# Optimization experiments

Hardware: AMD Instinct MI355X
Metric: run time of the kernel (lower is better)

Reference implementation:

```python
import jax, jax.numpy as jnp
import numpy as np

WS = 6        # window size -> N = 36 tokens per window
HEADS = 16

def _rel_index(ws):
    coords = np.stack(np.meshgrid(np.arange(ws), np.arange(ws), indexing='ij')).reshape(2, -1)
    rel = coords[:, :, None] - coords[:, None, :] + (ws - 1)
    return jnp.asarray(rel[0] * (2 * ws - 1) + rel[1])  # (N, N) int

REL_IDX = _rel_index(WS)

def _ln(x, g, b, eps=1e-5):
    m = x.mean(-1, keepdims=True)
    v = x.var(-1, keepdims=True)
    return (x - m) / jnp.sqrt(v + eps) * g + b

def setup_inputs() -> dict:
    key = jax.random.key(0)
    ks = jax.random.split(key, 6)
    B, H, W, C = 16, 96, 96, 512
    hid = 4 * C
    s = 0.02
    return {
        'x': jax.random.normal(ks[0], (B, H, W, C), jnp.float32),
        'w_qkv': jax.random.normal(ks[1], (C, 3 * C), jnp.float32) * s,
        'w_proj': jax.random.normal(ks[2], (C, C), jnp.float32) * s,
        'b_proj': jnp.zeros((C,), jnp.float32),
        'rel_bias': jax.random.normal(ks[3], ((2 * WS - 1) ** 2, HEADS), jnp.float32) * s,
        'ln1_g': jnp.ones((C,), jnp.float32), 'ln1_b': jnp.zeros((C,), jnp.float32),
        'ln2_g': jnp.ones((C,), jnp.float32), 'ln2_b': jnp.zeros((C,), jnp.float32),
        'w_fc1': jax.random.normal(ks[4], (C, hid), jnp.float32) * s,
        'b_fc1': jnp.zeros((hid,), jnp.float32),
        'w_fc2': jax.random.normal(ks[5], (hid, C), jnp.float32) * s,
        'b_fc2': jnp.zeros((C,), jnp.float32),
    }

def reference(x, w_qkv, w_proj, b_proj, rel_bias, ln1_g, ln1_b, ln2_g, ln2_b, w_fc1, b_fc1, w_fc2, b_fc2):
    B, H, W, C = x.shape
    h, d, N = HEADS, C // HEADS, WS * WS
    nh, nw = H // WS, W // WS
    # window partition: (B,H,W,C) -> (B*nh*nw, N, C)
    xw = x.reshape(B, nh, WS, nw, WS, C).transpose(0, 1, 3, 2, 4, 5).reshape(B * nh * nw, N, C)
    xn = _ln(xw, ln1_g, ln1_b)
    qkv = xn @ w_qkv
    q, k, v = jnp.split(qkv, 3, axis=-1)
    to_heads = lambda t: t.reshape(-1, N, h, d).transpose(0, 2, 1, 3)  # (B_, h, N, d)
    q = to_heads(q) * (d ** -0.5)
    k = to_heads(k)
    v = to_heads(v)
    attn = jnp.einsum('bhnd,bhmd->bhnm', q, k)
    bias = rel_bias[REL_IDX.reshape(-1)].reshape(N, N, h).transpose(2, 0, 1)  # (h, N, N)
    attn = jax.nn.softmax(attn + bias[None], axis=-1)
    o = jnp.einsum('bhnm,bhmd->bhnd', attn, v).transpose(0, 2, 1, 3).reshape(-1, N, C)
    o = o @ w_proj + b_proj
    # un-window; NOTE: source has no residual around attention (x is replaced)
    x2 = o.reshape(B, nh, nw, WS, WS, C).transpose(0, 1, 3, 2, 4, 5).reshape(B, H, W, C)
    xm = _ln(x2, ln2_g, ln2_b)
    mlp = jax.nn.gelu(xm @ w_fc1 + b_fc1, approximate=False) @ w_fc2 + b_fc2
    return x2 + mlp
```

## Files before the change

kernel.cpp:

```cpp
#include <hip/hip_runtime.h>
#include <stdint.h>

#define TOK 147456
#define CCH 512

typedef __attribute__((ext_vector_type(8))) short short8;
typedef __attribute__((ext_vector_type(4))) float f32x4;

struct alignas(8) US4 { unsigned short a, b, c, d; };

typedef __attribute__((address_space(3))) void lds_void;
typedef const __attribute__((address_space(1))) void gbl_void;

__device__ inline void gload16(const void* g, void* l) {
    __builtin_amdgcn_global_load_lds((gbl_void*)g, (lds_void*)l, 16, 0, 0);
}

__device__ inline unsigned short f2bf(float f) {
    union { float f; unsigned u; } v{f};
    unsigned r = v.u + 0x7fffu + ((v.u >> 16) & 1u);
    return (unsigned short)(r >> 16);
}
__device__ inline float bf2f(unsigned short h) {
    union { unsigned u; float f; } v; v.u = ((unsigned)h) << 16; return v.f;
}
__device__ inline float frcp(float x) {
    float r; asm("v_rcp_f32 %0, %1" : "=v"(r) : "v"(x)); return r;
}

__global__ void wprep(const float* __restrict__ in, unsigned short* __restrict__ out,
                      int K, int N) {
    int idx = blockIdx.x * 256 + threadIdx.x;
    if (idx >= K * N) return;
    int k = idx / N, n = idx % N;
    out[(size_t)n * K + k] = f2bf(in[idx]);
}

__global__ void biasprep(const float* __restrict__ rb, float* __restrict__ bb) {
    int idx = blockIdx.x * 256 + threadIdx.x;
    if (idx >= 16 * 48 * 48) return;
    int h = idx / 2304, rem = idx % 2304, r = rem / 48, c = rem % 48;
    float v = -1e9f;
    if (r < 36 && c < 36) {
        int dy = r / 6 - c / 6 + 5;
        int dx = r % 6 - c % 6 + 5;
        v = rb[(dy * 11 + dx) * 16 + h];
    }
    bb[idx] = v;
}

__global__ __launch_bounds__(256) void ln_k(const float* __restrict__ x,
                                            const float* __restrict__ g,
                                            const float* __restrict__ b,
                                            unsigned short* __restrict__ out, int ntok) {
    int lane = threadIdx.x & 63;
    int tok = blockIdx.x * 4 + (threadIdx.x >> 6);
    if (tok >= ntok) return;
    const float4* xr = (const float4*)(x + (size_t)tok * CCH);
    float4 v0 = xr[lane], v1 = xr[lane + 64];
    float s  = v0.x + v0.y + v0.z + v0.w + v1.x + v1.y + v1.z + v1.w;
    float s2 = v0.x*v0.x + v0.y*v0.y + v0.z*v0.z + v0.w*v0.w
             + v1.x*v1.x + v1.y*v1.y + v1.z*v1.z + v1.w*v1.w;
#pragma unroll
    for (int off = 32; off; off >>= 1) { s += __shfl_xor(s, off); s2 += __shfl_xor(s2, off); }
    float mean = s * (1.f / 512.f);
    float var  = s2 * (1.f / 512.f) - mean * mean;
    float inv  = rsqrtf(var + 1e-5f);
    const float4* gp = (const float4*)g;
    const float4* bp = (const float4*)b;
    float4 g0 = gp[lane], g1 = gp[lane + 64], b0 = bp[lane], b1 = bp[lane + 64];
    US4 o0, o1;
    o0.a = f2bf((v0.x - mean) * inv * g0.x + b0.x);
    o0.b = f2bf((v0.y - mean) * inv * g0.y + b0.y);
    o0.c = f2bf((v0.z - mean) * inv * g0.z + b0.z);
    o0.d = f2bf((v0.w - mean) * inv * g0.w + b0.w);
    o1.a = f2bf((v1.x - mean) * inv * g1.x + b1.x);
    o1.b = f2bf((v1.y - mean) * inv * g1.y + b1.y);
    o1.c = f2bf((v1.z - mean) * inv * g1.z + b1.z);
    o1.d = f2bf((v1.w - mean) * inv * g1.w + b1.w);
    unsigned short* op = out + (size_t)tok * CCH;
    *(US4*)(op + 4 * lane)       = o0;
    *(US4*)(op + 256 + 4 * lane) = o1;
}

__global__ __launch_bounds__(256) void ln_bf(const unsigned short* __restrict__ x,
                                             const float* __restrict__ g,
                                             const float* __restrict__ b,
                                             unsigned short* __restrict__ out, int ntok) {
    int lane = threadIdx.x & 63;
    int tok = blockIdx.x * 4 + (threadIdx.x >> 6);
    if (tok >= ntok) return;
    short8 v = *(const short8*)(x + (size_t)tok * CCH + lane * 8);
    float f[8];
#pragma unroll
    for (int j = 0; j < 8; ++j) f[j] = bf2f((unsigned short)v[j]);
    float s = 0.f, s2 = 0.f;
#pragma unroll
    for (int j = 0; j < 8; ++j) { s += f[j]; s2 += f[j] * f[j]; }
#pragma unroll
    for (int off = 32; off; off >>= 1) { s += __shfl_xor(s, off); s2 += __shfl_xor(s2, off); }
    float mean = s * (1.f / 512.f);
    float var  = s2 * (1.f / 512.f) - mean * mean;
    float inv  = rsqrtf(var + 1e-5f);
    const float4* gp = (const float4*)g + lane * 2;
    const float4* bp = (const float4*)b + lane * 2;
    float4 g0 = gp[0], g1 = gp[1], b0 = bp[0], b1 = bp[1];
    float gg[8] = {g0.x, g0.y, g0.z, g0.w, g1.x, g1.y, g1.z, g1.w};
    float bb[8] = {b0.x, b0.y, b0.z, b0.w, b1.x, b1.y, b1.z, b1.w};
    short8 o;
#pragma unroll
    for (int j = 0; j < 8; ++j) o[j] = (short)f2bf((f[j] - mean) * inv * gg[j] + bb[j]);
    *(short8*)(out + (size_t)tok * CCH + lane * 8) = o;
}

__global__ __launch_bounds__(256) void attn_mfma(const unsigned short* __restrict__ qkv,
                                                 const float* __restrict__ biasb,
                                                 unsigned short* __restrict__ o) {
    __shared__ __align__(16) unsigned short p_lds[4][48 * 64];
    __shared__ __align__(16) unsigned short v_lds[4][32 * 64];

    int tid  = threadIdx.x;
    int wv   = tid >> 6;
    int lane = tid & 63;
    int l15  = lane & 15;
    int g    = lane >> 4;

    int wid = blockIdx.x * 4 + wv;
    int h   = wid & 15;
    int win = wid >> 4;
    int img  = win >> 8;
    int wrow = (win >> 4) & 15;
    int wcol = win & 15;
    int tok_base = (img * 96 + wrow * 6) * 96 + wcol * 6;

    unsigned short* pw = p_lds[wv];
    unsigned short* vw = v_lds[wv];

    #define TOKOF(r) (tok_base + (r) + 90 * ((r) / 6))

    short8 z8 = {};
    for (int e = lane; e < 224; e += 64) {
        if (e < 128) {
            int ch = e >> 2, kst = 32 + (e & 3) * 8;
            *(short8*)(vw + ch * 64 + (kst ^ ((ch & 7) << 3))) = z8;
        } else {
            int ee = e - 128; int q = ee >> 1, kst = 48 + (ee & 1) * 8;
            *(short8*)(pw + q * 64 + (kst ^ ((q & 7) << 3))) = z8;
        }
    }

    for (int e = lane; e < 144; e += 64) {
        int r = e >> 2, c0 = (e & 3) * 8;
        short8 vv = *(const short8*)(qkv + (size_t)TOKOF(r) * 1536 + 1024 + h * 32 + c0);
#pragma unroll
        for (int j = 0; j < 8; ++j) {
            int ch = c0 + j;
            vw[ch * 64 + (r ^ ((ch & 7) << 3))] = (unsigned short)vv[j];
        }
    }

    short8 qf[3], kf[3];
#pragma unroll
    for (int t = 0; t < 3; ++t) {
        int r = t * 16 + l15;
        if (r < 36) {
            size_t ba = (size_t)TOKOF(r) * 1536 + h * 32 + g * 8;
            qf[t] = *(const short8*)(qkv + ba);
            kf[t] = *(const short8*)(qkv + ba + 512);
        } else { qf[t] = z8; kf[t] = z8; }
    }

    f32x4 s[3][3] = {};
#pragma unroll
    for (int mt = 0; mt < 3; ++mt)
#pragma unroll
        for (int nt = 0; nt < 3; ++nt)
            s[mt][nt] = __builtin_amdgcn_mfma_f32_16x16x32_bf16(qf[mt], kf[nt], s[mt][nt], 0, 0, 0);

    const float SCALE = 0.17677669529663687f;
    const float* bh = biasb + h * 2304;
#pragma unroll
    for (int mt = 0; mt < 3; ++mt) {
#pragma unroll
        for (int r = 0; r < 4; ++r) {
            int row = mt * 16 + g * 4 + r;
            const float* bb = bh + row * 48 + l15;
            float v0 = fmaf(s[mt][0][r], SCALE, bb[0]);
            float v1 = fmaf(s[mt][1][r], SCALE, bb[16]);
            float v2 = fmaf(s[mt][2][r], SCALE, bb[32]);
            float m = fmaxf(fmaxf(v0, v1), v2);
#pragma unroll
            for (int off = 1; off < 16; off <<= 1) m = fmaxf(m, __shfl_xor(m, off));
            float e0 = __expf(v0 - m), e1 = __expf(v1 - m), e2 = __expf(v2 - m);
            float sm = e0 + e1 + e2;
#pragma unroll
            for (int off = 1; off < 16; off <<= 1) sm += __shfl_xor(sm, off);
            float inv = 1.f / sm;
            int sw = (row & 7) << 3;
            unsigned short* pr = pw + row * 64;
            pr[(l15)      ^ sw] = f2bf(e0 * inv);
            pr[(16 + l15) ^ sw] = f2bf(e1 * inv);
            pr[(32 + l15) ^ sw] = f2bf(e2 * inv);
        }
    }

    f32x4 oacc[3][2] = {};
#pragma unroll
    for (int ks = 0; ks < 2; ++ks) {
        int kst = ks * 32 + g * 8;
        short8 bfr[2];
#pragma unroll
        for (int nt = 0; nt < 2; ++nt) {
            int c = nt * 16 + l15;
            bfr[nt] = *(const short8*)(vw + c * 64 + (kst ^ ((c & 7) << 3)));
        }
#pragma unroll
        for (int mt = 0; mt < 3; ++mt) {
            int q = mt * 16 + l15;
            short8 pa = *(const short8*)(pw + q * 64 + (kst ^ ((q & 7) << 3)));
#pragma unroll
            for (int nt = 0; nt < 2; ++nt)
                oacc[mt][nt] = __builtin_amdgcn_mfma_f32_16x16x32_bf16(pa, bfr[nt], oacc[mt][nt], 0, 0, 0);
        }
    }

#pragma unroll
    for (int mt = 0; mt < 3; ++mt) {
#pragma unroll
        for (int r = 0; r < 4; ++r) {
            int q = mt * 16 + g * 4 + r;
            if (q < 36) {
                size_t rb = (size_t)TOKOF(q) * 512 + h * 32;
#pragma unroll
                for (int nt = 0; nt < 2; ++nt)
                    o[rb + nt * 16 + l15] = f2bf(oacc[mt][nt][r]);
            }
        }
    }
    #undef TOKOF
}

template <int EPI>
__global__ __launch_bounds__(256, 4) void gemm8(const unsigned short* __restrict__ A,
                                                const unsigned short* __restrict__ Bt,
                                                int M, int N, int K,
                                                const float* __restrict__ bias,
                                                const unsigned short* __restrict__ resid,
                                                void* __restrict__ Cout) {
    extern __shared__ char lds[];
    int tid = threadIdx.x;
    int w = tid >> 6, lane = tid & 63;
    int l15 = lane & 15, grp = lane >> 4;
    int wm = w >> 1, wn = w & 1;

    int nbn = N >> 7;
    int nwg = gridDim.x;
    int q = nwg >> 3, r = nwg & 7;
    int xcd = blockIdx.x & 7, pos_ = blockIdx.x >> 3;
    int wgid = (xcd < r ? xcd * (q + 1) : r * (q + 1) + (xcd - r) * q) + pos_;
    int bm = wgid / nbn, bn = wgid % nbn;

    int NT = K >> 5;

    int u = (tid & 7) ^ ((tid >> 3) & 7);
    int srow = ((tid >> 3) << 1) + (u >> 2);
    int scol = (u & 3) * 8;
    const unsigned short* aSrc = A  + ((size_t)bm * 128 + srow) * (size_t)K + scol;
    const unsigned short* bSrc = Bt + ((size_t)bn * 128 + srow) * (size_t)K + scol;

    #define STAGE(t, sp) do { size_t ko_ = (size_t)(t) * 32; \
        gload16(aSrc + ko_,                  (sp) + tid * 16); \
        gload16(aSrc + ko_ + (size_t)64 * K, (sp) + 4096  + tid * 16); \
        gload16(bSrc + ko_,                  (sp) + 8192  + tid * 16); \
        gload16(bSrc + ko_ + (size_t)64 * K, (sp) + 12288 + tid * 16); } while (0)

    int rpos = (grp + (l15 & 1) * 4) ^ ((l15 >> 1) & 7);
    int aRd = (wm * 32 + (l15 >> 1)) * 128 + rpos * 16;
    int bRd = 8192 + (wn * 32 + (l15 >> 1)) * 128 + rpos * 16;

    f32x4 acc[4][4] = {};

    char* s0 = lds;
    char* s1 = lds + 16384;
    STAGE(0, s0);

    for (int t = 0; t < NT; ++t) {
        char* cur = (t & 1) ? s1 : s0;
        char* nxt = (t & 1) ? s0 : s1;
        if (t + 1 < NT) {
            STAGE(t + 1, nxt);
            asm volatile("s_waitcnt vmcnt(4)" ::: "memory");
        } else {
            asm volatile("s_waitcnt vmcnt(0)" ::: "memory");
        }
        __builtin_amdgcn_s_barrier();
        short8 af[4], bf[4];
#pragma unroll
        for (int m = 0; m < 4; ++m) af[m] = *(const short8*)(cur + aRd + m * 1024);
#pragma unroll
        for (int n = 0; n < 4; ++n) bf[n] = *(const short8*)(cur + bRd + n * 1024);
        asm volatile("s_waitcnt lgkmcnt(0)" ::: "memory");
        __builtin_amdgcn_sched_barrier(0);
        __builtin_amdgcn_s_setprio(1);
#pragma unroll
        for (int m = 0; m < 4; ++m)
#pragma unroll
            for (int n = 0; n < 4; ++n)
                acc[m][n] = __builtin_amdgcn_mfma_f32_16x16x32_bf16(af[m], bf[n], acc[m][n], 0, 0, 0);
        __builtin_amdgcn_s_setprio(0);
        __builtin_amdgcn_s_barrier();
    }
    #undef STAGE

    int row0 = bm * 128 + wm * 64 + grp * 4;
    int col0 = bn * 128 + wn * 64 + l15;
#pragma unroll
    for (int m = 0; m < 4; ++m) {
#pragma unroll
        for (int n = 0; n < 4; ++n) {
            int col = col0 + n * 16;
            float bv = (EPI == 0) ? 0.f : bias[col];
#pragma unroll
            for (int r2 = 0; r2 < 4; ++r2) {
                int row = row0 + m * 16 + r2;
                size_t idx = (size_t)row * N + col;
                float val = acc[m][n][r2] + bv;
                if (EPI == 0) {
                    ((unsigned short*)Cout)[idx] = f2bf(val);
                } else if (EPI == 1) {
                    ((unsigned short*)Cout)[idx] = f2bf(val);
                } else if (EPI == 2) {
                    float t1 = val * val;
                    float t2 = fmaf(t1, 0.0713548163f, 1.5957691216f);
                    float z  = val * t2;
                    float e  = __expf(z);
                    float rr = frcp(e + 1.f);
                    float ge = val - val * rr;
                    ((unsigned short*)Cout)[idx] = f2bf(ge);
                } else {
                    ((float*)Cout)[idx] = val + bf2f(resid[idx]);
                }
            }
        }
    }
}

extern "C" void kernel_launch(void* const* d_in, const int* in_sizes, int n_in,
                              void* d_out, int out_size, void* d_ws, size_t ws_size,
                              hipStream_t stream) {
    const float* x       = (const float*)d_in[0];
    const float* w_qkv   = (const float*)d_in[1];
    const float* w_proj  = (const float*)d_in[2];
    const float* b_proj  = (const float*)d_in[3];
    const float* relb    = (const float*)d_in[4];
    const float* ln1g    = (const float*)d_in[5];
    const float* ln1b    = (const float*)d_in[6];
    const float* ln2g    = (const float*)d_in[7];
    const float* ln2b    = (const float*)d_in[8];
    const float* w_fc1   = (const float*)d_in[9];
    const float* b_fc1   = (const float*)d_in[10];
    const float* w_fc2   = (const float*)d_in[11];
    const float* b_fc2   = (const float*)d_in[12];
    float* out = (float*)d_out;

    hipFuncSetAttribute(reinterpret_cast<const void*>(&gemm8<0>),
                        hipFuncAttributeMaxDynamicSharedMemorySize, 32768);
    hipFuncSetAttribute(reinterpret_cast<const void*>(&gemm8<1>),
                        hipFuncAttributeMaxDynamicSharedMemorySize, 32768);
    hipFuncSetAttribute(reinterpret_cast<const void*>(&gemm8<2>),
                        hipFuncAttributeMaxDynamicSharedMemorySize, 32768);
    hipFuncSetAttribute(reinterpret_cast<const void*>(&gemm8<3>),
                        hipFuncAttributeMaxDynamicSharedMemorySize, 32768);

    char* w = (char*)d_ws;
    unsigned short* wT_qkv  = (unsigned short*)w; w += (size_t)1536 * 512 * 2;
    unsigned short* wT_proj = (unsigned short*)w; w += (size_t)512  * 512 * 2;
    unsigned short* wT_fc1  = (unsigned short*)w; w += (size_t)2048 * 512 * 2;
    unsigned short* wT_fc2  = (unsigned short*)w; w += (size_t)512  * 2048 * 2;
    float* biasb            = (float*)w;          w += (size_t)16 * 48 * 48 * 4;
    size_t wbytes = (size_t)(w - (char*)d_ws);

    int nchunk = 16;
    for (int c = 1; c <= 16; c *= 2) {
        size_t tokc = TOK / c;
        if (wbytes + tokc * 6144 <= ws_size) { nchunk = c; break; }
    }
    size_t tokc = TOK / nchunk;
    unsigned short* buf1 = (unsigned short*)w;
    unsigned short* buf2 = (unsigned short*)(w + tokc * 1024);
    unsigned short* buf3 = (unsigned short*)(w + tokc * 5120);

    wprep<<<(512 * 1536 + 255) / 256, 256, 0, stream>>>(w_qkv,  wT_qkv,  512, 1536);
    wprep<<<(512 * 512  + 255) / 256, 256, 0, stream>>>(w_proj, wT_proj, 512, 512);
    wprep<<<(512 * 2048 + 255) / 256, 256, 0, stream>>>(w_fc1,  wT_fc1,  512, 2048);
    wprep<<<(2048 * 512 + 255) / 256, 256, 0, stream>>>(w_fc2,  wT_fc2,  2048, 512);
    biasprep<<<(16 * 48 * 48 + 255) / 256, 256, 0, stream>>>(relb, biasb);

    int Mc = (int)tokc;
    int gm = Mc / 128;
    int imgs = Mc / 9216;

    for (int c = 0; c < nchunk; ++c) {
        size_t toff = (size_t)c * tokc;
        const float* xc = x + toff * CCH;
        float* outc = out + toff * CCH;

        ln_k<<<Mc / 4, 256, 0, stream>>>(xc, ln1g, ln1b, buf1, Mc);
        gemm8<0><<<gm * 12, 256, 32768, stream>>>(buf1, wT_qkv, Mc, 1536, 512,
                                                  nullptr, nullptr, buf2);
        attn_mfma<<<imgs * 1024, 256, 0, stream>>>(buf2, biasb, buf1);
        gemm8<1><<<gm * 4, 256, 32768, stream>>>(buf1, wT_proj, Mc, 512, 512,
                                                 b_proj, nullptr, buf3);
        ln_bf<<<Mc / 4, 256, 0, stream>>>(buf3, ln2g, ln2b, buf1, Mc);
        gemm8<2><<<gm * 16, 256, 32768, stream>>>(buf1, wT_fc1, Mc, 2048, 512,
                                                  b_fc1, nullptr, buf2);
        gemm8<3><<<gm * 4, 256, 32768, stream>>>(buf2, wT_fc2, Mc, 512, 2048,
                                                 b_fc2, buf3, outc);
    }
}
```

Measured before the change: 1.654 ms.

## Rewrite GEMM as 256x256 tile, 8-wave, 8-phase pipelined MFMA kernel

Replaces the 128x128, 4-wave double-buffered GEMM with a 256x256 tile computed by 8 waves. The kernel uses 128 KB of LDS split into two K-halves of 64 each, and its loop is split into eight phases that interleave global_load_lds prefetches with quadrant MFMA blocks. The goal is higher arithmetic intensity per byte loaded and hiding global-load latency behind MFMA work. In exchange, occupancy drops to one workgroup per CU and the grid shrinks, so the smaller GEMMs may be short of parallelism and register pressure from the 8x4 accumulators rises.

```diff
diff --git a/kernel.cpp b/kernel.cpp
--- a/kernel.cpp
+++ b/kernel.cpp
@@ -241,7 +241,7 @@
 }
 
 template <int EPI>
-__global__ __launch_bounds__(256, 4) void gemm8(const unsigned short* __restrict__ A,
+__global__ __launch_bounds__(512, 1) void gemm8(const unsigned short* __restrict__ A,
                                                 const unsigned short* __restrict__ Bt,
                                                 int M, int N, int K,
                                                 const float* __restrict__ bias,
@@ -250,72 +250,108 @@
     extern __shared__ char lds[];
     int tid = threadIdx.x;
     int w = tid >> 6, lane = tid & 63;
-    int l15 = lane & 15, grp = lane >> 4;
-    int wm = w >> 1, wn = w & 1;
-
-    int nbn = N >> 7;
+    int l15 = lane & 15, grp = lane >> 4, l7 = l15 & 7;
+    int wm = w >> 2, wn = w & 3;
+
+    int nbn = N >> 8;
     int nwg = gridDim.x;
     int q = nwg >> 3, r = nwg & 7;
     int xcd = blockIdx.x & 7, pos_ = blockIdx.x >> 3;
     int wgid = (xcd < r ? xcd * (q + 1) : r * (q + 1) + (xcd - r) * q) + pos_;
     int bm = wgid / nbn, bn = wgid % nbn;
 
-    int NT = K >> 5;
-
-    int u = (tid & 7) ^ ((tid >> 3) & 7);
-    int srow = ((tid >> 3) << 1) + (u >> 2);
-    int scol = (u & 3) * 8;
-    const unsigned short* aSrc = A  + ((size_t)bm * 128 + srow) * (size_t)K + scol;
-    const unsigned short* bSrc = Bt + ((size_t)bn * 128 + srow) * (size_t)K + scol;
-
-    #define STAGE(t, sp) do { size_t ko_ = (size_t)(t) * 32; \
-        gload16(aSrc + ko_,                  (sp) + tid * 16); \
-        gload16(aSrc + ko_ + (size_t)64 * K, (sp) + 4096  + tid * 16); \
-        gload16(bSrc + ko_,                  (sp) + 8192  + tid * 16); \
-        gload16(bSrc + ko_ + (size_t)64 * K, (sp) + 12288 + tid * 16); } while (0)
-
-    int rpos = (grp + (l15 & 1) * 4) ^ ((l15 >> 1) & 7);
-    int aRd = (wm * 32 + (l15 >> 1)) * 128 + rpos * 16;
-    int bRd = 8192 + (wn * 32 + (l15 >> 1)) * 128 + rpos * 16;
-
-    f32x4 acc[4][4] = {};
-
-    char* s0 = lds;
-    char* s1 = lds + 16384;
-    STAGE(0, s0);
-
-    for (int t = 0; t < NT; ++t) {
-        char* cur = (t & 1) ? s1 : s0;
-        char* nxt = (t & 1) ? s0 : s1;
-        if (t + 1 < NT) {
-            STAGE(t + 1, nxt);
+    int NI = K >> 7;
+
+    int trow = tid >> 3;
+    int sg = (tid & 7) ^ (trow & 7);
+    const unsigned short* aBase = A  + ((size_t)bm * 256 + trow) * (size_t)K + sg * 8;
+    const unsigned short* bBase = Bt + ((size_t)bn * 256 + trow) * (size_t)K + sg * 8;
+
+    #define STG(base, rowOff, kt, dst) do { \
+        gload16((base) + (size_t)(rowOff) * K + (kt),        lds + (dst) + tid * 16); \
+        gload16((base) + (size_t)((rowOff) + 64) * K + (kt), lds + (dst) + 8192 + tid * 16); } while (0)
+
+    int aR0 = wm * 16384 + l15 * 128 + ((grp ^ l7) << 4);
+    int bR0 = 32768 + (wn >> 1) * 16384 + (wn & 1) * 8192 + l15 * 128 + ((grp ^ l7) << 4);
+
+    f32x4 acc[8][4] = {};
+    short8 Af[4][2], Bf[4][2];
+
+    STG(bBase, 0,   0,  32768);
+    STG(bBase, 128, 0,  32768 + 16384);
+    STG(aBase, 0,   0,  0);
+    STG(aBase, 128, 0,  16384);
+    STG(bBase, 0,   64, 65536 + 32768);
+    STG(bBase, 128, 64, 65536 + 32768 + 16384);
+    asm volatile("s_waitcnt vmcnt(4)" ::: "memory");
+    __builtin_amdgcn_s_barrier();
+
+    #define RDA(d, qm) do { int ab_ = (d) * 65536 + (qm) * 8192 + aR0; \
+        _Pragma("unroll") for (int mi_ = 0; mi_ < 4; ++mi_) { \
+            Af[mi_][0] = *(const short8*)(lds + ab_ + mi_ * 2048); \
+            Af[mi_][1] = *(const short8*)(lds + ((ab_ + mi_ * 2048) ^ 64)); } } while (0)
+    #define RDB(d, nh) do { int bb_ = (d) * 65536 + (nh) * 4096 + bR0; \
+        _Pragma("unroll") for (int nj_ = 0; nj_ < 2; ++nj_) { \
+            Bf[(nh) * 2 + nj_][0] = *(const short8*)(lds + bb_ + nj_ * 2048); \
+            Bf[(nh) * 2 + nj_][1] = *(const short8*)(lds + ((bb_ + nj_ * 2048) ^ 64)); } } while (0)
+    #define MFQ(qm, nh) do { \
+        _Pragma("unroll") for (int mi_ = 0; mi_ < 4; ++mi_) \
+        _Pragma("unroll") for (int nj_ = 0; nj_ < 2; ++nj_) \
+        _Pragma("unroll") for (int ks_ = 0; ks_ < 2; ++ks_) \
+            acc[(qm) * 4 + mi_][(nh) * 2 + nj_] = __builtin_amdgcn_mfma_f32_16x16x32_bf16( \
+                Af[mi_][ks_], Bf[(nh) * 2 + nj_][ks_], acc[(qm) * 4 + mi_][(nh) * 2 + nj_], 0, 0, 0); } while (0)
+    #define PH_PRE  do { __builtin_amdgcn_s_barrier(); \
+        asm volatile("s_waitcnt lgkmcnt(0)" ::: "memory"); \
+        __builtin_amdgcn_sched_barrier(0); \
+        __builtin_amdgcn_s_setprio(1); } while (0)
+    #define PH_POST do { __builtin_amdgcn_s_setprio(0); \
+        __builtin_amdgcn_s_barrier(); } while (0)
+
+    for (int i = 0; i < NI; ++i) {
+        int tka = i << 7, tkb = tka + 64;
+        bool pf = (i + 1 < NI);
+        RDA(0, 0); RDB(0, 0);
+        STG(aBase, 0, tkb, 65536);
+        PH_PRE; MFQ(0, 0); PH_POST;
+        RDB(0, 1);
+        STG(aBase, 128, tkb, 65536 + 16384);
+        PH_PRE; MFQ(0, 1); PH_POST;
+        RDA(0, 1);
+        if (pf) STG(bBase, 0, tka + 128, 32768);
+        PH_PRE; MFQ(1, 0); PH_POST;
+        if (pf) {
+            STG(bBase, 128, tka + 128, 32768 + 16384);
             asm volatile("s_waitcnt vmcnt(4)" ::: "memory");
         } else {
             asm volatile("s_waitcnt vmcnt(0)" ::: "memory");
         }
-        __builtin_amdgcn_s_barrier();
-        short8 af[4], bf[4];
-#pragma unroll
-        for (int m = 0; m < 4; ++m) af[m] = *(const short8*)(cur + aRd + m * 1024);
-#pragma unroll
-        for (int n = 0; n < 4; ++n) bf[n] = *(const short8*)(cur + bRd + n * 1024);
-        asm volatile("s_waitcnt lgkmcnt(0)" ::: "memory");
-        __builtin_amdgcn_sched_barrier(0);
-        __builtin_amdgcn_s_setprio(1);
-#pragma unroll
-        for (int m = 0; m < 4; ++m)
-#pragma unroll
-            for (int n = 0; n < 4; ++n)
-                acc[m][n] = __builtin_amdgcn_mfma_f32_16x16x32_bf16(af[m], bf[n], acc[m][n], 0, 0, 0);
-        __builtin_amdgcn_s_setprio(0);
-        __builtin_amdgcn_s_barrier();
-    }
-    #undef STAGE
-
-    int row0 = bm * 128 + wm * 64 + grp * 4;
-    int col0 = bn * 128 + wn * 64 + l15;
-#pragma unroll
-    for (int m = 0; m < 4; ++m) {
+        PH_PRE; MFQ(1, 1); PH_POST;
+        RDA(1, 0); RDB(1, 0);
+        if (pf) STG(aBase, 0, tka + 128, 0);
+        PH_PRE; MFQ(0, 0); PH_POST;
+        RDB(1, 1);
+        if (pf) STG(aBase, 128, tka + 128, 16384);
+        PH_PRE; MFQ(0, 1); PH_POST;
+        RDA(1, 1);
+        if (pf) STG(bBase, 0, tkb + 128, 65536 + 32768);
+        PH_PRE; MFQ(1, 0); PH_POST;
+        if (pf) {
+            STG(bBase, 128, tkb + 128, 65536 + 32768 + 16384);
+            asm volatile("s_waitcnt vmcnt(4)" ::: "memory");
+        }
+        PH_PRE; MFQ(1, 1); PH_POST;
+    }
+    #undef STG
+    #undef RDA
+    #undef RDB
+    #undef MFQ
+    #undef PH_PRE
+    #undef PH_POST
+
+    int row0 = bm * 256 + wm * 128 + grp * 4;
+    int col0 = bn * 256 + wn * 64 + l15;
+#pragma unroll
+    for (int m = 0; m < 8; ++m) {
 #pragma unroll
         for (int n = 0; n < 4; ++n) {
             int col = col0 + n * 16;
@@ -364,13 +400,13 @@
     float* out = (float*)d_out;
 
     hipFuncSetAttribute(reinterpret_cast<const void*>(&gemm8<0>),
-                        hipFuncAttributeMaxDynamicSharedMemorySize, 32768);
+                        hipFuncAttributeMaxDynamicSharedMemorySize, 131072);
     hipFuncSetAttribute(reinterpret_cast<const void*>(&gemm8<1>),
-                        hipFuncAttributeMaxDynamicSharedMemorySize, 32768);
+                        hipFuncAttributeMaxDynamicSharedMemorySize, 131072);
     hipFuncSetAttribute(reinterpret_cast<const void*>(&gemm8<2>),
-                        hipFuncAttributeMaxDynamicSharedMemorySize, 32768);
+                        hipFuncAttributeMaxDynamicSharedMemorySize, 131072);
     hipFuncSetAttribute(reinterpret_cast<const void*>(&gemm8<3>),
-                        hipFuncAttributeMaxDynamicSharedMemorySize, 32768);
+                        hipFuncAttributeMaxDynamicSharedMemorySize, 131072);
 
     char* w = (char*)d_ws;
     unsigned short* wT_qkv  = (unsigned short*)w; w += (size_t)1536 * 512 * 2;
@@ -397,7 +433,7 @@
     biasprep<<<(16 * 48 * 48 + 255) / 256, 256, 0, stream>>>(relb, biasb);
 
     int Mc = (int)tokc;
-    int gm = Mc / 128;
+    int gm = Mc / 256;
     int imgs = Mc / 9216;
 
     for (int c = 0; c < nchunk; ++c) {
@@ -406,15 +442,15 @@
         float* outc = out + toff * CCH;
 
         ln_k<<<Mc / 4, 256, 0, stream>>>(xc, ln1g, ln1b, buf1, Mc);
-        gemm8<0><<<gm * 12, 256, 32768, stream>>>(buf1, wT_qkv, Mc, 1536, 512,
+        gemm8<0><<<gm * 6, 512, 131072, stream>>>(buf1, wT_qkv, Mc, 1536, 512,
                                                   nullptr, nullptr, buf2);
         attn_mfma<<<imgs * 1024, 256, 0, stream>>>(buf2, biasb, buf1);
-        gemm8<1><<<gm * 4, 256, 32768, stream>>>(buf1, wT_proj, Mc, 512, 512,
-                                                 b_proj, nullptr, buf3);
+        gemm8<1><<<gm * 2, 512, 131072, stream>>>(buf1, wT_proj, Mc, 512, 512,
+                                                  b_proj, nullptr, buf3);
         ln_bf<<<Mc / 4, 256, 0, stream>>>(buf3, ln2g, ln2b, buf1, Mc);
-        gemm8<2><<<gm * 16, 256, 32768, stream>>>(buf1, wT_fc1, Mc, 2048, 512,
+        gemm8<2><<<gm * 8, 512, 131072, stream>>>(buf1, wT_fc1, Mc, 2048, 512,
                                                   b_fc1, nullptr, buf2);
-        gemm8<3><<<gm * 4, 256, 32768, stream>>>(buf2, wT_fc2, Mc, 512, 2048,
-                                                 b_fc2, buf3, outc);
-    }
-}
+        gemm8<3><<<gm * 2, 512, 131072, stream>>>(buf2, wT_fc2, Mc, 512, 2048,
+                                                  b_fc2, buf3, outc);
+    }
+}
```

New measurement: 1.508 ms, median of 3. -8.8%, faster.
